# Optimization experiments

Hardware: AMD Instinct MI355X
Metric: run time of the kernel (lower is better)

The kernel has to match this reference:

```python
import jax, jax.numpy as jnp
import numpy as np

B, S, HID = 2, 2048, 2048
H, D = 16, 128        # num_heads, kv_channels
LAYER_IDX = 4
MASK_VALUE = -10000.0


def setup_inputs() -> dict:
    key = jax.random.key(0)
    ks = jax.random.split(key, 5)
    hidden_states = jax.random.normal(ks[0], (B, S, HID), dtype=jnp.float32)
    # causal mask, broadcastable to [B, q, H, k] per torch.where(mask, w, mask_value)
    causal = jnp.tril(jnp.ones((S, S), dtype=bool))
    attention_mask = jnp.broadcast_to(causal[None, :, None, :], (B, S, 1, S))
    Wq = jax.random.normal(ks[1], (HID, H * D), dtype=jnp.float32) * (HID ** -0.5)
    bq = jnp.zeros((H * D,), dtype=jnp.float32)
    Wkv = jax.random.normal(ks[2], (HID, 2 * D), dtype=jnp.float32) * (HID ** -0.5)
    bkv = jnp.zeros((2 * D,), dtype=jnp.float32)
    Wp = jax.random.normal(ks[3], (H * D, HID), dtype=jnp.float32) * ((H * D) ** -0.5)
    bp = jnp.zeros((HID,), dtype=jnp.float32)
    return {"hidden_states": hidden_states, "attention_mask": attention_mask,
            "Wq": Wq, "bq": bq, "Wkv": Wkv, "bkv": bkv, "Wp": Wp, "bp": bp}


def reference(hidden_states, attention_mask, Wq, bq, Wkv, bkv, Wp, bp):
    # projections
    q = hidden_states @ Wq + bq                      # [B,S,H*D]
    kv = hidden_states @ Wkv + bkv                   # [B,S,2D]
    k, v = kv[..., :D], kv[..., D:]                  # shared single K/V head [B,S,D]
    qh = q.reshape(B, S, H, D)
    # baddbmm with alpha = 1/(layer_idx * sqrt(D))
    scale_factor = (1.0 / LAYER_IDX) / (D ** 0.5)
    scores = jnp.einsum('bqhd,bkd->bqhk', qh, k) * scale_factor  # [B,q,H,k]
    # upcast softmax with unscale = layer_idx, masked with -1e4
    scores = scores.astype(jnp.float32) * LAYER_IDX
    scores = jnp.where(attention_mask, scores, MASK_VALUE)
    weights = jax.nn.softmax(scores, axis=-1).astype(hidden_states.dtype)
    attn = jnp.einsum('bqhk,bkd->bqhd', weights, v).reshape(B, S, H * D)
    out = attn @ Wp + bp
    return out
```

## Files before the change

### kernel.cpp

```cpp
#include <hip/hip_runtime.h>

#define DEVI __device__ __forceinline__

typedef unsigned int u32;
typedef unsigned short u16;

constexpr int Bc = 2, Sc = 2048, HIDc = 2048, Hc = 16, Dc = 128;
constexpr int Mrows = Bc * Sc;
constexpr float SCALE = 0.08838834764831845f;
constexpr float M0 = 16.0f;

typedef float f32x4 __attribute__((ext_vector_type(4)));
typedef __bf16 bf16x8 __attribute__((ext_vector_type(8)));

DEVI float bf2f(u16 v) { return __builtin_bit_cast(float, (u32)v << 16); }
DEVI u16 f2bf(float x) {
  u32 u = __builtin_bit_cast(u32, x);
  u32 r = (u + 0x7fffu + ((u >> 16) & 1u)) >> 16;
  return (u16)r;
}

DEVI void async16(void* lds, const void* g) {
  __builtin_amdgcn_global_load_lds((const __attribute__((address_space(1))) void*)g,
                                   (__attribute__((address_space(3))) void*)lds,
                                   16, 0, 0);
}

constexpr int PRE_BLOCKS = 6289;
constexpr int TS = 66;

DEVI void do_transpose64(const void* in, u16* out, int R, int C, int c0, int r0, bool bf,
                         u16* tile, int tid) {
  const int cg = (tid & 7) * 8, ry = tid >> 3;
#pragma unroll
  for (int p = 0; p < 2; ++p) {
    int r = ry + p * 32;
    size_t idx = (size_t)(r0 + r) * C + (c0 + cg);
    u16 tmp[8];
    if (bf) {
      *(uint4*)tmp = *(const uint4*)&((const u16*)in)[idx];
    } else {
      const float* f = (const float*)in + idx;
#pragma unroll
      for (int j = 0; j < 8; ++j) tmp[j] = f2bf(f[j]);
    }
    *(uint4*)&tile[r * TS + cg] = *(const uint4*)tmp;
  }
  __syncthreads();
  const int rx = (tid & 7) * 8, cy = tid >> 3;
#pragma unroll
  for (int p = 0; p < 2; ++p) {
    int c = cy + p * 32;
    u16 tmp[8];
#pragma unroll
    for (int j = 0; j < 8; ++j) tmp[j] = tile[(rx + j) * TS + c];
    *(uint4*)&out[(size_t)(c0 + c) * R + r0 + rx] = *(const uint4*)tmp;
  }
}

__global__ __launch_bounds__(256) void pre_kernel(const void* __restrict__ hs,
                                                  const void* __restrict__ Wq,
                                                  const void* __restrict__ bq,
                                                  const void* __restrict__ Wkv,
                                                  const void* __restrict__ bkv,
                                                  const void* __restrict__ Wp,
                                                  const void* __restrict__ bp,
                                                  u16* __restrict__ HSb, u16* __restrict__ WqT,
                                                  u16* __restrict__ WkvT, u16* __restrict__ WpT,
                                                  u16* __restrict__ biasB, int* __restrict__ flag) {
  __shared__ int cnt;
  __shared__ u16 tile[64 * TS];
  const int tid = threadIdx.x, bx = blockIdx.x;
  if (tid == 0) cnt = 0;
  __syncthreads();
  int ok = 0;
  const u32* hw = (const u32*)hs;
  for (int i = tid; i < 512; i += 256) {
    u32 lo = hw[i] & 0xffffu;
    u32 e = (lo >> 7) & 0xffu;
    if (lo == 0u || (e >= 118u && e <= 134u)) ok++;
  }
  atomicAdd(&cnt, ok);
  __syncthreads();
  const bool bf = cnt > 256;
  if (bx == 0 && tid == 0) *flag = bf ? 1 : 0;

  if (bx < 4096) {
    int i = (bx * 256 + tid) * 8;
    if (bf) {
      *(uint4*)&HSb[i] = *(const uint4*)&((const u16*)hs)[i];
    } else {
      const float* f = (const float*)hs;
      u16 tmp[8];
#pragma unroll
      for (int j = 0; j < 8; ++j) tmp[j] = f2bf(f[i + j]);
      *(uint4*)&HSb[i] = *(const uint4*)tmp;
    }
  } else if (bx < 5120) {
    int t = bx - 4096;
    do_transpose64(Wq, WqT, 2048, 2048, (t & 31) * 64, (t >> 5) * 64, bf, tile, tid);
  } else if (bx < 5248) {
    int t = bx - 5120;
    do_transpose64(Wkv, WkvT, 2048, 256, (t & 3) * 64, (t >> 2) * 64, bf, tile, tid);
  } else if (bx < 6272) {
    int t = bx - 5248;
    do_transpose64(Wp, WpT, 2048, 2048, (t & 31) * 64, (t >> 5) * 64, bf, tile, tid);
  } else {
    int i = (bx - 6272) * 256 + tid;
    if (i < 4352) {
      const void* src;
      int j;
      if (i < 2048) { src = bq; j = i; }
      else if (i < 2304) { src = bkv; j = i - 2048; }
      else { src = bp; j = i - 2304; }
      biasB[i] = bf ? ((const u16*)src)[j] : f2bf(((const float*)src)[j]);
    }
  }
}

__global__ __launch_bounds__(512, 4) void gemm_bt(const u16* __restrict__ A,
                                                  const u16* __restrict__ BT,
                                                  const u16* __restrict__ bias,
                                                  void* __restrict__ C,
                                                  int M, int N, int K,
                                                  const int* __restrict__ flag,
                                                  int mode) {
  __shared__ __align__(16) u16 As[2][128 * 32];
  __shared__ __align__(16) u16 Bs[2][128 * 32];
  const int tid = threadIdx.x;
  const int bm = blockIdx.x, bn = blockIdx.y;
  const int wave = tid >> 6, lane = tid & 63;
  const int wm = (wave & 3) * 32, wn = (wave >> 2) * 64;
  const int lr = lane & 15, kq = lane >> 4;
  f32x4 acc[2][4] = {};
  const size_t a_base = (size_t)bm * 128 * K;
  const size_t b_base = (size_t)bn * 128 * K;

#define STAGE(k0, buf)                                                             \
  {                                                                                \
    int r = tid >> 2, c = tid & 3;                                                 \
    int gc = (c ^ (r & 3)) << 3;                                                   \
    async16(&As[buf][tid * 8], A + a_base + (size_t)r * K + (k0) + gc);            \
    async16(&Bs[buf][tid * 8], BT + b_base + (size_t)r * K + (k0) + gc);           \
  }

  STAGE(0, 0);
  const int nsteps = K >> 5;
  for (int s = 0; s < nsteps; ++s) {
    const int cur = s & 1;
    asm volatile("s_waitcnt vmcnt(0)" ::: "memory");
    asm volatile("s_barrier" ::: "memory");
    if (s + 1 < nsteps) STAGE((s + 1) << 5, cur ^ 1);
    bf16x8 af[2], bfr[4];
#pragma unroll
    for (int i = 0; i < 2; ++i) {
      int ra = wm + i * 16 + lr;
      af[i] = *(const bf16x8*)&As[cur][ra * 32 + ((kq ^ (ra & 3)) << 3)];
    }
#pragma unroll
    for (int i = 0; i < 4; ++i) {
      int rb = wn + i * 16 + lr;
      bfr[i] = *(const bf16x8*)&Bs[cur][rb * 32 + ((kq ^ (rb & 3)) << 3)];
    }
#pragma unroll
    for (int mi = 0; mi < 2; ++mi)
#pragma unroll
      for (int ni = 0; ni < 4; ++ni)
        acc[mi][ni] = __builtin_amdgcn_mfma_f32_16x16x32_bf16(af[mi], bfr[ni], acc[mi][ni], 0, 0, 0);
  }
#undef STAGE

  if (mode == 3) {
    u16* Qout = (u16*)C;
    u16* KsG = Qout + (size_t)4096 * 2048;
    u16* VtG = KsG + (size_t)4096 * 128;
    const bool isQ = (bn < 16);
#pragma unroll
    for (int mi = 0; mi < 2; ++mi)
#pragma unroll
      for (int ni = 0; ni < 4; ++ni) {
        int col = bn * 128 + wn + ni * 16 + lr;
        float bv = bf2f(bias[col]);
#pragma unroll
        for (int rr = 0; rr < 4; ++rr) {
          int row = bm * 128 + wm + mi * 16 + kq * 4 + rr;
          u16 v = f2bf(acc[mi][ni][rr] + bv);
          if (isQ) {
            Qout[(size_t)row * 2048 + col] = v;
          } else {
            int c2 = col - 2048;
            if (c2 < 128) {
              int d = c2;
              KsG[(size_t)row * 128 + (((d >> 3) ^ (row & 15)) << 3) + (d & 7)] = v;
            } else {
              int d = c2 - 128, bb = row >> 11, s = row & 2047;
              VtG[((size_t)(bb * 128 + d)) * 2048 + (s & ~63) +
                  ((((s >> 3) & 7) ^ (d & 7)) << 3) + (s & 7)] = v;
            }
          }
        }
      }
    return;
  }
  const bool out16 = (mode == 0) || (*flag != 0);
#pragma unroll
  for (int mi = 0; mi < 2; ++mi)
#pragma unroll
    for (int ni = 0; ni < 4; ++ni) {
      int col = bn * 128 + wn + ni * 16 + lr;
      float bv = bf2f(bias[col]);
#pragma unroll
      for (int rr = 0; rr < 4; ++rr) {
        int row = bm * 128 + wm + mi * 16 + kq * 4 + rr;
        float v = acc[mi][ni][rr] + bv;
        size_t idx = (size_t)row * N + col;
        if (out16) ((u16*)C)[idx] = f2bf(v);
        else ((float*)C)[idx] = v;
      }
    }
}

constexpr int PS_STRIDE = 72;

__global__ __launch_bounds__(256, 1) void flash_mfma(const u16* __restrict__ Q,
                                                     const u16* __restrict__ KsG,
                                                     const u16* __restrict__ VtG,
                                                     u16* __restrict__ O) {
  __shared__ __align__(16) u16 Ks[2][64 * 128];
  __shared__ __align__(16) u16 Vt[2][128 * 64];
  __shared__ __align__(16) u16 Ps[128 * PS_STRIDE];
  const int pairidx = blockIdx.x, h = blockIdx.y, b = blockIdx.z;
  const int tid = threadIdx.x;
  const int wave = tid >> 6, lane = tid & 63;
  const int lr = lane & 15, kq = lane >> 4;
  const int wm = wave * 32;

  for (int half = 0; half < 2; ++half) {
    const int qt = (half == 0) ? pairidx : 15 - pairidx;
    bf16x8 qf[2][4];
#pragma unroll
    for (int mi = 0; mi < 2; ++mi) {
      const u16* qbase =
          Q + ((size_t)(b * 2048 + qt * 128 + wm + mi * 16 + lr)) * 2048 + h * 128;
#pragma unroll
      for (int kk = 0; kk < 4; ++kk)
        qf[mi][kk] = *(const bf16x8*)(qbase + kk * 32 + kq * 8);
    }
    f32x4 of[2][8] = {};
    float lsum[2][4] = {{0.f, 0.f, 0.f, 0.f}, {0.f, 0.f, 0.f, 0.f}};
    const int srow = qt * 128 + wm + kq * 4;
    const int kmax = qt * 128 + 64;
    const int diag0 = qt * 128;

    {
      const u16* g = KsG + ((size_t)(b * 2048)) * 128;
#pragma unroll
      for (int it = 0; it < 4; ++it)
        async16(&Ks[0][it * 2048 + tid * 8], g + it * 2048 + tid * 8);
      const size_t vbase = ((size_t)b * 128) * 2048;
#pragma unroll
      for (int it = 0; it < 4; ++it) {
        int chunk = it * 256 + tid;
        async16(&Vt[0][chunk * 8], VtG + vbase + (size_t)(chunk >> 3) * 2048 + (chunk & 7) * 8);
      }
    }

    for (int k0 = 0; k0 <= kmax; k0 += 64) {
      const int cur = (k0 >> 6) & 1;
      asm volatile("s_waitcnt vmcnt(0)" ::: "memory");
      asm volatile("s_barrier" ::: "memory");
      if (k0 + 64 <= kmax) {
        const int nxt = cur ^ 1;
        const u16* g = KsG + ((size_t)(b * 2048 + k0 + 64)) * 128;
#pragma unroll
        for (int it = 0; it < 4; ++it)
          async16(&Ks[nxt][it * 2048 + tid * 8], g + it * 2048 + tid * 8);
        const size_t vbase = ((size_t)b * 128) * 2048 + k0 + 64;
#pragma unroll
        for (int it = 0; it < 4; ++it) {
          int chunk = it * 256 + tid;
          async16(&Vt[nxt][chunk * 8],
                  VtG + vbase + (size_t)(chunk >> 3) * 2048 + (chunk & 7) * 8);
        }
      }

      const bool diag = (k0 >= diag0);
      f32x4 sf[2][4] = {};
#pragma unroll
      for (int nt = 0; nt < 4; ++nt) {
        int keyl = nt * 16 + lr;
#pragma unroll
        for (int kk = 0; kk < 4; ++kk) {
          const bf16x8 kf = *(const bf16x8*)&Ks[cur][keyl * 128 + ((((kk << 2) + kq) ^ lr) << 3)];
          sf[0][nt] = __builtin_amdgcn_mfma_f32_16x16x32_bf16(qf[0][kk], kf, sf[0][nt], 0, 0, 0);
          sf[1][nt] = __builtin_amdgcn_mfma_f32_16x16x32_bf16(qf[1][kk], kf, sf[1][nt], 0, 0, 0);
        }
      }
#pragma unroll
      for (int mi = 0; mi < 2; ++mi)
#pragma unroll
        for (int nt = 0; nt < 4; ++nt) {
          int t = k0 + nt * 16 + lr;
#pragma unroll
          for (int r = 0; r < 4; ++r) {
            float v = fmaf(sf[mi][nt][r], SCALE, -M0);
            if (diag && t > srow + mi * 16 + r) v = -1e30f;
            float p = __expf(v);
            lsum[mi][r] += p;
            Ps[(wm + mi * 16 + kq * 4 + r) * PS_STRIDE + nt * 16 + lr] = f2bf(p);
          }
        }
#pragma unroll
      for (int ks = 0; ks < 2; ++ks) {
        const bf16x8 pf0 = *(const bf16x8*)&Ps[(wm + lr) * PS_STRIDE + ks * 32 + kq * 8];
        const bf16x8 pf1 = *(const bf16x8*)&Ps[(wm + 16 + lr) * PS_STRIDE + ks * 32 + kq * 8];
#pragma unroll
        for (int dt = 0; dt < 8; ++dt) {
          int d = dt * 16 + lr;
          const bf16x8 vf = *(const bf16x8*)&Vt[cur][d * 64 + ((((ks << 2) + kq) ^ (d & 7)) << 3)];
          of[0][dt] = __builtin_amdgcn_mfma_f32_16x16x32_bf16(pf0, vf, of[0][dt], 0, 0, 0);
          of[1][dt] = __builtin_amdgcn_mfma_f32_16x16x32_bf16(pf1, vf, of[1][dt], 0, 0, 0);
        }
      }
    }
#pragma unroll
    for (int mi = 0; mi < 2; ++mi) {
      float linv[4];
#pragma unroll
      for (int r = 0; r < 4; ++r) {
        float l = lsum[mi][r];
        l += __shfl_xor(l, 1);
        l += __shfl_xor(l, 2);
        l += __shfl_xor(l, 4);
        l += __shfl_xor(l, 8);
        linv[r] = 1.f / l;
      }
      u16* obase =
          O + ((size_t)(b * 2048 + qt * 128 + wm + mi * 16 + kq * 4)) * 2048 + h * 128;
#pragma unroll
      for (int dt = 0; dt < 8; ++dt)
#pragma unroll
        for (int r = 0; r < 4; ++r)
          obase[(size_t)r * 2048 + dt * 16 + lr] = f2bf(of[mi][dt][r] * linv[r]);
    }
    __syncthreads();
  }
}

extern "C" void kernel_launch(void* const* d_in, const int* in_sizes, int n_in,
                              void* d_out, int out_size, void* d_ws, size_t ws_size,
                              hipStream_t stream) {
  (void)in_sizes; (void)n_in; (void)out_size; (void)ws_size;
  const void* hs  = d_in[0];
  const void* Wq  = d_in[2];
  const void* bq  = d_in[3];
  const void* Wkv = d_in[4];
  const void* bkv = d_in[5];
  const void* Wp  = d_in[6];
  const void* bp  = d_in[7];

  char* ws = (char*)d_ws;
  int* flag  = (int*)(ws + 0);
  u16* HSb   = (u16*)(ws + 256);
  u16* WqT   = (u16*)(ws + 16777472);
  u16* WkvT  = (u16*)(ws + 25166080);
  u16* WpT   = (u16*)(ws + 26214656);
  u16* biasB = (u16*)(ws + 34603264);
  u16* Qb    = (u16*)(ws + 34611968);
  u16* KsG   = (u16*)(ws + 51389184);
  u16* VtG   = (u16*)(ws + 52437760);
  u16* ATTNb = (u16*)(ws + 53486336);

  pre_kernel<<<PRE_BLOCKS, 256, 0, stream>>>(hs, Wq, bq, Wkv, bkv, Wp, bp,
                                             HSb, WqT, WkvT, WpT, biasB, flag);
  gemm_bt<<<dim3(32, 18), 512, 0, stream>>>(HSb, WqT, biasB, Qb, 4096, 2304, 2048, flag, 3);
  flash_mfma<<<dim3(8, 16, 2), 256, 0, stream>>>(Qb, KsG, VtG, ATTNb);
  gemm_bt<<<dim3(32, 16), 512, 0, stream>>>(ATTNb, WpT, biasB + 2304, d_out, 4096, 2048, 2048, flag, 1);
}
```

Measured before the change: 328.2 us.

## Split flash attention work across 8 waves along key and head-dim axes

Doubles the attention block to 512 threads. Waves are split into 4 row groups and 2 column groups: each column group computes half the key columns of the score tile and half of the output head dimension. A barrier is added between writing the shared P tile and reading it, and the row sums are reduced across the two column groups through shared memory before normalisation. This aims to raise wave occupancy and latency hiding with only 256 blocks in the grid, at the cost of an extra barrier per key tile.

```diff
diff --git a/kernel.cpp b/kernel.cpp
--- a/kernel.cpp
+++ b/kernel.cpp
@@ -222,18 +222,20 @@
 
 constexpr int PS_STRIDE = 72;
 
-__global__ __launch_bounds__(256, 1) void flash_mfma(const u16* __restrict__ Q,
+__global__ __launch_bounds__(512, 2) void flash_mfma(const u16* __restrict__ Q,
                                                      const u16* __restrict__ KsG,
                                                      const u16* __restrict__ VtG,
                                                      u16* __restrict__ O) {
   __shared__ __align__(16) u16 Ks[2][64 * 128];
   __shared__ __align__(16) u16 Vt[2][128 * 64];
   __shared__ __align__(16) u16 Ps[128 * PS_STRIDE];
+  __shared__ float Lred[2][128];
   const int pairidx = blockIdx.x, h = blockIdx.y, b = blockIdx.z;
   const int tid = threadIdx.x;
   const int wave = tid >> 6, lane = tid & 63;
   const int lr = lane & 15, kq = lane >> 4;
-  const int wm = wave * 32;
+  const int mg = wave & 3, ng = wave >> 2;
+  const int wm = mg * 32;
 
   for (int half = 0; half < 2; ++half) {
     const int qt = (half == 0) ? pairidx : 15 - pairidx;
@@ -246,7 +248,7 @@
       for (int kk = 0; kk < 4; ++kk)
         qf[mi][kk] = *(const bf16x8*)(qbase + kk * 32 + kq * 8);
     }
-    f32x4 of[2][8] = {};
+    f32x4 of[2][4] = {};
     float lsum[2][4] = {{0.f, 0.f, 0.f, 0.f}, {0.f, 0.f, 0.f, 0.f}};
     const int srow = qt * 128 + wm + kq * 4;
     const int kmax = qt * 128 + 64;
@@ -255,12 +257,12 @@
     {
       const u16* g = KsG + ((size_t)(b * 2048)) * 128;
 #pragma unroll
-      for (int it = 0; it < 4; ++it)
-        async16(&Ks[0][it * 2048 + tid * 8], g + it * 2048 + tid * 8);
+      for (int it = 0; it < 2; ++it)
+        async16(&Ks[0][it * 4096 + tid * 8], g + it * 4096 + tid * 8);
       const size_t vbase = ((size_t)b * 128) * 2048;
 #pragma unroll
-      for (int it = 0; it < 4; ++it) {
-        int chunk = it * 256 + tid;
+      for (int it = 0; it < 2; ++it) {
+        int chunk = it * 512 + tid;
         async16(&Vt[0][chunk * 8], VtG + vbase + (size_t)(chunk >> 3) * 2048 + (chunk & 7) * 8);
       }
     }
@@ -273,22 +275,22 @@
         const int nxt = cur ^ 1;
         const u16* g = KsG + ((size_t)(b * 2048 + k0 + 64)) * 128;
 #pragma unroll
-        for (int it = 0; it < 4; ++it)
-          async16(&Ks[nxt][it * 2048 + tid * 8], g + it * 2048 + tid * 8);
+        for (int it = 0; it < 2; ++it)
+          async16(&Ks[nxt][it * 4096 + tid * 8], g + it * 4096 + tid * 8);
         const size_t vbase = ((size_t)b * 128) * 2048 + k0 + 64;
 #pragma unroll
-        for (int it = 0; it < 4; ++it) {
-          int chunk = it * 256 + tid;
+        for (int it = 0; it < 2; ++it) {
+          int chunk = it * 512 + tid;
           async16(&Vt[nxt][chunk * 8],
                   VtG + vbase + (size_t)(chunk >> 3) * 2048 + (chunk & 7) * 8);
         }
       }
 
       const bool diag = (k0 >= diag0);
-      f32x4 sf[2][4] = {};
-#pragma unroll
-      for (int nt = 0; nt < 4; ++nt) {
-        int keyl = nt * 16 + lr;
+      f32x4 sf[2][2] = {};
+#pragma unroll
+      for (int nt = 0; nt < 2; ++nt) {
+        int keyl = ng * 32 + nt * 16 + lr;
 #pragma unroll
         for (int kk = 0; kk < 4; ++kk) {
           const bf16x8 kf = *(const bf16x8*)&Ks[cur][keyl * 128 + ((((kk << 2) + kq) ^ lr) << 3)];
@@ -299,24 +301,27 @@
 #pragma unroll
       for (int mi = 0; mi < 2; ++mi)
 #pragma unroll
-        for (int nt = 0; nt < 4; ++nt) {
-          int t = k0 + nt * 16 + lr;
+        for (int nt = 0; nt < 2; ++nt) {
+          int t = k0 + ng * 32 + nt * 16 + lr;
 #pragma unroll
           for (int r = 0; r < 4; ++r) {
             float v = fmaf(sf[mi][nt][r], SCALE, -M0);
             if (diag && t > srow + mi * 16 + r) v = -1e30f;
             float p = __expf(v);
             lsum[mi][r] += p;
-            Ps[(wm + mi * 16 + kq * 4 + r) * PS_STRIDE + nt * 16 + lr] = f2bf(p);
+            Ps[(wm + mi * 16 + kq * 4 + r) * PS_STRIDE + ng * 32 + nt * 16 + lr] = f2bf(p);
           }
         }
+      asm volatile("s_waitcnt lgkmcnt(0)" ::: "memory");
+      asm volatile("s_barrier" ::: "memory");
+      __builtin_amdgcn_sched_barrier(0);
 #pragma unroll
       for (int ks = 0; ks < 2; ++ks) {
         const bf16x8 pf0 = *(const bf16x8*)&Ps[(wm + lr) * PS_STRIDE + ks * 32 + kq * 8];
         const bf16x8 pf1 = *(const bf16x8*)&Ps[(wm + 16 + lr) * PS_STRIDE + ks * 32 + kq * 8];
 #pragma unroll
-        for (int dt = 0; dt < 8; ++dt) {
-          int d = dt * 16 + lr;
+        for (int dt = 0; dt < 4; ++dt) {
+          int d = ng * 64 + dt * 16 + lr;
           const bf16x8 vf = *(const bf16x8*)&Vt[cur][d * 64 + ((((ks << 2) + kq) ^ (d & 7)) << 3)];
           of[0][dt] = __builtin_amdgcn_mfma_f32_16x16x32_bf16(pf0, vf, of[0][dt], 0, 0, 0);
           of[1][dt] = __builtin_amdgcn_mfma_f32_16x16x32_bf16(pf1, vf, of[1][dt], 0, 0, 0);
@@ -324,8 +329,7 @@
       }
     }
 #pragma unroll
-    for (int mi = 0; mi < 2; ++mi) {
-      float linv[4];
+    for (int mi = 0; mi < 2; ++mi)
 #pragma unroll
       for (int r = 0; r < 4; ++r) {
         float l = lsum[mi][r];
@@ -333,12 +337,28 @@
         l += __shfl_xor(l, 2);
         l += __shfl_xor(l, 4);
         l += __shfl_xor(l, 8);
-        linv[r] = 1.f / l;
-      }
-      u16* obase =
-          O + ((size_t)(b * 2048 + qt * 128 + wm + mi * 16 + kq * 4)) * 2048 + h * 128;
-#pragma unroll
-      for (int dt = 0; dt < 8; ++dt)
+        lsum[mi][r] = l;
+      }
+    if (lr == 0) {
+#pragma unroll
+      for (int mi = 0; mi < 2; ++mi)
+#pragma unroll
+        for (int r = 0; r < 4; ++r)
+          Lred[ng][wm + mi * 16 + kq * 4 + r] = lsum[mi][r];
+    }
+    __syncthreads();
+#pragma unroll
+    for (int mi = 0; mi < 2; ++mi) {
+      float linv[4];
+#pragma unroll
+      for (int r = 0; r < 4; ++r) {
+        int row = wm + mi * 16 + kq * 4 + r;
+        linv[r] = 1.f / (Lred[0][row] + Lred[1][row]);
+      }
+      u16* obase = O + ((size_t)(b * 2048 + qt * 128 + wm + mi * 16 + kq * 4)) * 2048 +
+                   h * 128 + ng * 64;
+#pragma unroll
+      for (int dt = 0; dt < 4; ++dt)
 #pragma unroll
         for (int r = 0; r < 4; ++r)
           obase[(size_t)r * 2048 + dt * 16 + lr] = f2bf(of[mi][dt][r] * linv[r]);
@@ -374,6 +394,6 @@
   pre_kernel<<<PRE_BLOCKS, 256, 0, stream>>>(hs, Wq, bq, Wkv, bkv, Wp, bp,
                                              HSb, WqT, WkvT, WpT, biasB, flag);
   gemm_bt<<<dim3(32, 18), 512, 0, stream>>>(HSb, WqT, biasB, Qb, 4096, 2304, 2048, flag, 3);
-  flash_mfma<<<dim3(8, 16, 2), 256, 0, stream>>>(Qb, KsG, VtG, ATTNb);
+  flash_mfma<<<dim3(8, 16, 2), 512, 0, stream>>>(Qb, KsG, VtG, ATTNb);
   gemm_bt<<<dim3(32, 16), 512, 0, stream>>>(ATTNb, WpT, biasB + 2304, d_out, 4096, 2048, 2048, flag, 1);
 }
```

After: 313.6 us. -4.4%, faster.

## Split flash attention into one q-tile per block with 32-key steps

Applied to the files above, without the earlier changes.

The flash attention kernel no longer processes a pair of query tiles (qt and 15-qt) per block. It now launches one block per query tile, reversing the tile order for batch 1 to balance load. The key/value tile shrinks from 64 to 32 keys, with a new V swizzle. Per-wave skipping of fully masked key steps is added and launch_bounds now allows 2 blocks per CU. The aim is more parallelism, higher occupancy and less wasted causal work, at the cost of more barriers per key and less MFMA work between syncs.

```diff
diff --git a/kernel.cpp b/kernel.cpp
--- a/kernel.cpp
+++ b/kernel.cpp
@@ -220,130 +220,122 @@
     }
 }
 
-constexpr int PS_STRIDE = 72;
-
-__global__ __launch_bounds__(256, 1) void flash_mfma(const u16* __restrict__ Q,
+constexpr int PS40 = 40;
+
+__global__ __launch_bounds__(256, 2) void flash_mfma(const u16* __restrict__ Q,
                                                      const u16* __restrict__ KsG,
                                                      const u16* __restrict__ VtG,
                                                      u16* __restrict__ O) {
-  __shared__ __align__(16) u16 Ks[2][64 * 128];
-  __shared__ __align__(16) u16 Vt[2][128 * 64];
-  __shared__ __align__(16) u16 Ps[128 * PS_STRIDE];
-  const int pairidx = blockIdx.x, h = blockIdx.y, b = blockIdx.z;
+  __shared__ __align__(16) u16 Ks[2][32 * 128];
+  __shared__ __align__(16) u16 Vt[2][128 * 32];
+  __shared__ __align__(16) u16 Ps[128 * PS40];
+  const int bx = blockIdx.x, h = blockIdx.y, b = blockIdx.z;
+  const int qt = b ? (15 - bx) : bx;
   const int tid = threadIdx.x;
   const int wave = tid >> 6, lane = tid & 63;
   const int lr = lane & 15, kq = lane >> 4;
   const int wm = wave * 32;
 
-  for (int half = 0; half < 2; ++half) {
-    const int qt = (half == 0) ? pairidx : 15 - pairidx;
-    bf16x8 qf[2][4];
-#pragma unroll
-    for (int mi = 0; mi < 2; ++mi) {
-      const u16* qbase =
-          Q + ((size_t)(b * 2048 + qt * 128 + wm + mi * 16 + lr)) * 2048 + h * 128;
-#pragma unroll
-      for (int kk = 0; kk < 4; ++kk)
-        qf[mi][kk] = *(const bf16x8*)(qbase + kk * 32 + kq * 8);
-    }
-    f32x4 of[2][8] = {};
-    float lsum[2][4] = {{0.f, 0.f, 0.f, 0.f}, {0.f, 0.f, 0.f, 0.f}};
-    const int srow = qt * 128 + wm + kq * 4;
-    const int kmax = qt * 128 + 64;
-    const int diag0 = qt * 128;
-
-    {
-      const u16* g = KsG + ((size_t)(b * 2048)) * 128;
-#pragma unroll
-      for (int it = 0; it < 4; ++it)
-        async16(&Ks[0][it * 2048 + tid * 8], g + it * 2048 + tid * 8);
-      const size_t vbase = ((size_t)b * 128) * 2048;
-#pragma unroll
-      for (int it = 0; it < 4; ++it) {
-        int chunk = it * 256 + tid;
-        async16(&Vt[0][chunk * 8], VtG + vbase + (size_t)(chunk >> 3) * 2048 + (chunk & 7) * 8);
-      }
-    }
-
-    for (int k0 = 0; k0 <= kmax; k0 += 64) {
-      const int cur = (k0 >> 6) & 1;
-      asm volatile("s_waitcnt vmcnt(0)" ::: "memory");
-      asm volatile("s_barrier" ::: "memory");
-      if (k0 + 64 <= kmax) {
-        const int nxt = cur ^ 1;
-        const u16* g = KsG + ((size_t)(b * 2048 + k0 + 64)) * 128;
-#pragma unroll
-        for (int it = 0; it < 4; ++it)
-          async16(&Ks[nxt][it * 2048 + tid * 8], g + it * 2048 + tid * 8);
-        const size_t vbase = ((size_t)b * 128) * 2048 + k0 + 64;
-#pragma unroll
-        for (int it = 0; it < 4; ++it) {
-          int chunk = it * 256 + tid;
-          async16(&Vt[nxt][chunk * 8],
-                  VtG + vbase + (size_t)(chunk >> 3) * 2048 + (chunk & 7) * 8);
-        }
-      }
-
-      const bool diag = (k0 >= diag0);
-      f32x4 sf[2][4] = {};
-#pragma unroll
-      for (int nt = 0; nt < 4; ++nt) {
+  bf16x8 qf[2][4];
+#pragma unroll
+  for (int mi = 0; mi < 2; ++mi) {
+    const u16* qbase =
+        Q + ((size_t)(b * 2048 + qt * 128 + wm + mi * 16 + lr)) * 2048 + h * 128;
+#pragma unroll
+    for (int kk = 0; kk < 4; ++kk)
+      qf[mi][kk] = *(const bf16x8*)(qbase + kk * 32 + kq * 8);
+  }
+  f32x4 of[2][8] = {};
+  float lsum[2][4] = {{0.f, 0.f, 0.f, 0.f}, {0.f, 0.f, 0.f, 0.f}};
+  const int rowbase = qt * 128 + wm;
+  const int nsteps = qt * 4 + 4;
+
+#define STAGEKV(t, buf)                                                              \
+  {                                                                                  \
+    const int k0s = (t) * 32;                                                        \
+    const u16* gk = KsG + ((size_t)(b * 2048 + k0s)) * 128;                          \
+    async16(&Ks[buf][tid * 8], gk + tid * 8);                                        \
+    async16(&Ks[buf][2048 + tid * 8], gk + 2048 + tid * 8);                          \
+    const int h4 = (k0s >> 3) & 4;                                                   \
+    const size_t vb = ((size_t)b * 128) * 2048;                                      \
+    _Pragma("unroll")                                                                \
+    for (int it = 0; it < 2; ++it) {                                                 \
+      int ch = it * 256 + tid;                                                       \
+      int d = ch >> 2, q = ch & 3;                                                   \
+      async16(&Vt[buf][ch * 8],                                                      \
+              VtG + vb + (size_t)d * 2048 + (k0s & ~63) + ((h4 ^ (d & 4)) + q) * 8); \
+    }                                                                                \
+  }
+
+  STAGEKV(0, 0);
+  for (int t = 0; t < nsteps; ++t) {
+    const int cur = t & 1;
+    const int k0 = t * 32;
+    asm volatile("s_waitcnt vmcnt(0)" ::: "memory");
+    asm volatile("s_barrier" ::: "memory");
+    if (t + 1 < nsteps) STAGEKV(t + 1, cur ^ 1);
+
+    const bool active = (k0 <= rowbase + 31);
+    if (active) {
+      f32x4 sf[2][2] = {};
+#pragma unroll
+      for (int nt = 0; nt < 2; ++nt) {
         int keyl = nt * 16 + lr;
 #pragma unroll
         for (int kk = 0; kk < 4; ++kk) {
-          const bf16x8 kf = *(const bf16x8*)&Ks[cur][keyl * 128 + ((((kk << 2) + kq) ^ lr) << 3)];
+          const bf16x8 kf =
+              *(const bf16x8*)&Ks[cur][keyl * 128 + ((((kk << 2) + kq) ^ lr) << 3)];
           sf[0][nt] = __builtin_amdgcn_mfma_f32_16x16x32_bf16(qf[0][kk], kf, sf[0][nt], 0, 0, 0);
           sf[1][nt] = __builtin_amdgcn_mfma_f32_16x16x32_bf16(qf[1][kk], kf, sf[1][nt], 0, 0, 0);
         }
       }
+      const bool diag = (k0 + 31 > rowbase);
 #pragma unroll
       for (int mi = 0; mi < 2; ++mi)
 #pragma unroll
-        for (int nt = 0; nt < 4; ++nt) {
-          int t = k0 + nt * 16 + lr;
+        for (int nt = 0; nt < 2; ++nt) {
+          int tkey = k0 + nt * 16 + lr;
 #pragma unroll
           for (int r = 0; r < 4; ++r) {
             float v = fmaf(sf[mi][nt][r], SCALE, -M0);
-            if (diag && t > srow + mi * 16 + r) v = -1e30f;
+            if (diag && tkey > rowbase + mi * 16 + kq * 4 + r) v = -1e30f;
             float p = __expf(v);
             lsum[mi][r] += p;
-            Ps[(wm + mi * 16 + kq * 4 + r) * PS_STRIDE + nt * 16 + lr] = f2bf(p);
+            Ps[(wm + mi * 16 + kq * 4 + r) * PS40 + nt * 16 + lr] = f2bf(p);
           }
         }
-#pragma unroll
-      for (int ks = 0; ks < 2; ++ks) {
-        const bf16x8 pf0 = *(const bf16x8*)&Ps[(wm + lr) * PS_STRIDE + ks * 32 + kq * 8];
-        const bf16x8 pf1 = *(const bf16x8*)&Ps[(wm + 16 + lr) * PS_STRIDE + ks * 32 + kq * 8];
-#pragma unroll
-        for (int dt = 0; dt < 8; ++dt) {
-          int d = dt * 16 + lr;
-          const bf16x8 vf = *(const bf16x8*)&Vt[cur][d * 64 + ((((ks << 2) + kq) ^ (d & 7)) << 3)];
-          of[0][dt] = __builtin_amdgcn_mfma_f32_16x16x32_bf16(pf0, vf, of[0][dt], 0, 0, 0);
-          of[1][dt] = __builtin_amdgcn_mfma_f32_16x16x32_bf16(pf1, vf, of[1][dt], 0, 0, 0);
-        }
+      const bf16x8 pf0 = *(const bf16x8*)&Ps[(wm + lr) * PS40 + kq * 8];
+      const bf16x8 pf1 = *(const bf16x8*)&Ps[(wm + 16 + lr) * PS40 + kq * 8];
+#pragma unroll
+      for (int dt = 0; dt < 8; ++dt) {
+        int d = dt * 16 + lr;
+        const bf16x8 vf = *(const bf16x8*)&Vt[cur][d * 32 + ((kq ^ (d & 3)) << 3)];
+        of[0][dt] = __builtin_amdgcn_mfma_f32_16x16x32_bf16(pf0, vf, of[0][dt], 0, 0, 0);
+        of[1][dt] = __builtin_amdgcn_mfma_f32_16x16x32_bf16(pf1, vf, of[1][dt], 0, 0, 0);
       }
     }
-#pragma unroll
-    for (int mi = 0; mi < 2; ++mi) {
-      float linv[4];
-#pragma unroll
-      for (int r = 0; r < 4; ++r) {
-        float l = lsum[mi][r];
-        l += __shfl_xor(l, 1);
-        l += __shfl_xor(l, 2);
-        l += __shfl_xor(l, 4);
-        l += __shfl_xor(l, 8);
-        linv[r] = 1.f / l;
-      }
-      u16* obase =
-          O + ((size_t)(b * 2048 + qt * 128 + wm + mi * 16 + kq * 4)) * 2048 + h * 128;
-#pragma unroll
-      for (int dt = 0; dt < 8; ++dt)
-#pragma unroll
-        for (int r = 0; r < 4; ++r)
-          obase[(size_t)r * 2048 + dt * 16 + lr] = f2bf(of[mi][dt][r] * linv[r]);
-    }
-    __syncthreads();
+  }
+#undef STAGEKV
+
+#pragma unroll
+  for (int mi = 0; mi < 2; ++mi) {
+    float linv[4];
+#pragma unroll
+    for (int r = 0; r < 4; ++r) {
+      float l = lsum[mi][r];
+      l += __shfl_xor(l, 1);
+      l += __shfl_xor(l, 2);
+      l += __shfl_xor(l, 4);
+      l += __shfl_xor(l, 8);
+      linv[r] = 1.f / l;
+    }
+    u16* obase =
+        O + ((size_t)(b * 2048 + qt * 128 + wm + mi * 16 + kq * 4)) * 2048 + h * 128;
+#pragma unroll
+    for (int dt = 0; dt < 8; ++dt)
+#pragma unroll
+      for (int r = 0; r < 4; ++r)
+        obase[(size_t)r * 2048 + dt * 16 + lr] = f2bf(of[mi][dt][r] * linv[r]);
   }
 }
 
@@ -374,6 +366,6 @@
   pre_kernel<<<PRE_BLOCKS, 256, 0, stream>>>(hs, Wq, bq, Wkv, bkv, Wp, bp,
                                              HSb, WqT, WkvT, WpT, biasB, flag);
   gemm_bt<<<dim3(32, 18), 512, 0, stream>>>(HSb, WqT, biasB, Qb, 4096, 2304, 2048, flag, 3);
-  flash_mfma<<<dim3(8, 16, 2), 256, 0, stream>>>(Qb, KsG, VtG, ATTNb);
+  flash_mfma<<<dim3(16, 16, 2), 256, 0, stream>>>(Qb, KsG, VtG, ATTNb);
   gemm_bt<<<dim3(32, 16), 512, 0, stream>>>(ATTNb, WpT, biasB + 2304, d_out, 4096, 2048, 2048, flag, 1);
 }
```

New measurement: 345.2 us. 1.05x slower.
